# Kernel tuning notes

Measured on AMD Instinct MI355X. Metric: run time of the kernel, lower is better.

Reference implementation:

```python
import jax, jax.numpy as jnp
import numpy as np

D = 2048
N_HID = 512
ATT = 512
BATCH = 256
L = 196


def setup_inputs() -> dict:
    key = jax.random.key(0)
    ks = jax.random.split(key, 8)
    s = 0.02
    return {
        "feature": jax.random.normal(ks[0], (BATCH, L, D), dtype=jnp.float32),
        "prev_h": jax.random.normal(ks[1], (BATCH, N_HID), dtype=jnp.float32),
        "W_enc": jax.random.normal(ks[2], (D, ATT), dtype=jnp.float32) * s,
        "b_enc": jnp.zeros((ATT,), dtype=jnp.float32),
        "W_dec": jax.random.normal(ks[3], (N_HID, ATT), dtype=jnp.float32) * s,
        "b_dec": jnp.zeros((ATT,), dtype=jnp.float32),
        "W_tot": jax.random.normal(ks[4], (ATT, 1), dtype=jnp.float32) * s,
        "b_tot": jnp.zeros((1,), dtype=jnp.float32),
    }


def reference(feature, prev_h, W_enc, b_enc, W_dec, b_dec, W_tot, b_tot):
    # att1: (N, L, A); att2: (N, A)
    att1 = jnp.einsum("nld,da->nla", feature, W_enc) + b_enc
    att2 = prev_h @ W_dec + b_dec
    att = jax.nn.relu(att1 + att2[:, None, :])          # (N, L, A)
    scores = (att @ W_tot)[..., 0] + b_tot[0]           # (N, L)
    alpha = jax.nn.softmax(scores, axis=1)              # (N, L)
    weighted_feature = jnp.einsum("nld,nl->nd", feature, alpha)  # (N, D)
    return weighted_feature, alpha
```

## Files before the change

kernel.cpp:

```cpp
#include <hip/hip_runtime.h>
#include <hip/hip_bf16.h>


typedef unsigned short u16;
typedef __attribute__((ext_vector_type(8))) short short8;
typedef __attribute__((ext_vector_type(4))) float f32x4;

#define BATCH 256
#define LQ    196
#define DDIM  2048
#define ADIM  512
#define MTOT  (BATCH * LQ)
#define WF_N  (BATCH * DDIM)
#define KQP   1032

__device__ __forceinline__ u16 bfc(float f) {
  return __builtin_bit_cast(u16, (__bf16)f);
}

__device__ __forceinline__ ushort4 cvt4(float4 f) {
  ushort4 r;
  r.x = bfc(f.x); r.y = bfc(f.y); r.z = bfc(f.z); r.w = bfc(f.w);
  return r;
}

__device__ __forceinline__ void glds16(const u16* g, u16* l) {
  __builtin_amdgcn_global_load_lds(
      (const __attribute__((address_space(1))) unsigned int*)g,
      (__attribute__((address_space(3))) unsigned int*)l, 16, 0, 0);
}

__global__ void prep_k(const float* __restrict__ W_enc, u16* __restrict__ Bst,
                       const float* __restrict__ prev_h,
                       const float* __restrict__ W_dec,
                       const float* __restrict__ b_dec,
                       const float* __restrict__ b_enc,
                       float* __restrict__ att2,
                       float* __restrict__ scores) {
  const int b = blockIdx.x, tid = threadIdx.x;
  __shared__ u16 smem[32 * 520];
  if (b < 64) {
    const int ks = b;
    for (int i4 = tid; i4 < 4096; i4 += 256) {
      int dl = i4 >> 7;
      int nn = (i4 & 127) << 2;
      float4 f = *(const float4*)(W_enc + (size_t)(ks * 32 + dl) * 512 + nn);
      *(ushort4*)(&smem[dl * 520 + nn]) = cvt4(f);
    }
    __syncthreads();
    for (int idx = tid; idx < 16384; idx += 256) {
      int kq = idx >> 12;
      int n  = (idx >> 3) & 511;
      int e  = idx & 7;
      Bst[(size_t)ks * 16384 + idx] = smem[(kq * 8 + e) * 520 + n];
    }
  } else if (b < 576) {
    const int n  = (b - 64) >> 1;
    const int c0 = ((b - 64) & 1) << 8;
    float* ph = (float*)smem;
    ph[tid]       = prev_h[n * 512 + tid];
    ph[tid + 256] = prev_h[n * 512 + tid + 256];
    __syncthreads();
    float a0 = b_dec[c0 + tid] + b_enc[c0 + tid];
    #pragma unroll 8
    for (int h = 0; h < 512; h++)
      a0 = fmaf(ph[h], W_dec[h * 512 + c0 + tid], a0);
    att2[n * 512 + c0 + tid] = a0;
  } else {
    scores[(b - 576) * 256 + tid] = 0.f;
  }
}

__global__ __launch_bounds__(256, 3) void score_gemm_k(
    const float* __restrict__ feature, const u16* __restrict__ Bst,
    const float* __restrict__ att2, const float* __restrict__ W_tot,
    float* __restrict__ scores) {
  __shared__ __align__(16) u16 sA[2][4 * KQP];
  __shared__ __align__(16) u16 sB[4][4 * KQP];
  __shared__ float sRed[2][128];

  const int tid = threadIdx.x;
  const int b = blockIdx.x;
  const int mt = (b >> 5) * 8 + (b & 7);
  const int nt = (b >> 3) & 3;
  const int r0 = mt << 7, n0 = nt << 7;
  const int wid = tid >> 6, lane = tid & 63;
  const int wgm = wid >> 1, wgn = wid & 1;
  const int quad = lane >> 4, cid = lane & 15;

  const int arow = tid >> 3, akk4 = tid & 7;
  const float* gA = feature + (size_t)(r0 + arow) * 2048 + akk4 * 4;
  const int wAoff = (akk4 >> 1) * KQP + (arow << 3) + ((akk4 & 1) << 2);

  const u16* gBlane = Bst + (size_t)wid * 4096 + ((size_t)n0 << 3) + lane * 8;

  const int abase = quad * KQP + (((wgm << 6) + cid) << 3);
  const int bbase = quad * KQP + (((wgn << 6) + cid) << 3);

  f32x4 zero = {0.f, 0.f, 0.f, 0.f};
  f32x4 acc[4][4];
  #pragma unroll
  for (int i = 0; i < 4; i++)
    #pragma unroll
    for (int j = 0; j < 4; j++) acc[i][j] = zero;

  float4 aS0_0, aS0_1, aS0_2, aS0_3;
  float4 aS1_0, aS1_1, aS1_2, aS1_3;
  float4 aS2_0, aS2_1, aS2_2, aS2_3;

#define LOAD_A(SET, KS) do {                                              \
    const float* p_ = gA + (size_t)(KS) * 32;                             \
    aS##SET##_0 = *(const float4*)(p_);                                   \
    aS##SET##_1 = *(const float4*)(p_ + 32 * 2048);                       \
    aS##SET##_2 = *(const float4*)(p_ + 64 * 2048);                       \
    aS##SET##_3 = *(const float4*)(p_ + 96 * 2048);                       \
  } while (0)

#define STAGE_A(SET, ABUF) do {                                           \
    u16* wa_ = &sA[ABUF][wAoff];                                          \
    *(ushort4*)(wa_)       = cvt4(aS##SET##_0);                           \
    *(ushort4*)(wa_ + 256) = cvt4(aS##SET##_1);                           \
    *(ushort4*)(wa_ + 512) = cvt4(aS##SET##_2);                           \
    *(ushort4*)(wa_ + 768) = cvt4(aS##SET##_3);                           \
  } while (0)

#define GLDS_B2(KS, BUFI) do {                                            \
    const u16* src_ = gBlane + (size_t)(KS) * 16384;                      \
    u16* dst_ = &sB[BUFI][wid * KQP];                                     \
    glds16(src_, dst_);                                                   \
    glds16(src_ + 512, dst_ + 512);                                       \
  } while (0)

#define COMPUTE(ABUF, BBUF) do {                                          \
    const u16* sa_ = &sA[ABUF][abase];                                    \
    const u16* sb_ = &sB[BBUF][bbase];                                    \
    short8 af_[4], bf_[4];                                                \
    _Pragma("unroll")                                                     \
    for (int mi = 0; mi < 4; mi++)                                        \
      af_[mi] = *(const short8*)(sa_ + (mi << 7));                        \
    _Pragma("unroll")                                                     \
    for (int ni = 0; ni < 4; ni++)                                        \
      bf_[ni] = *(const short8*)(sb_ + (ni << 7));                        \
    _Pragma("unroll")                                                     \
    for (int mi = 0; mi < 4; mi++)                                        \
      _Pragma("unroll")                                                   \
      for (int ni = 0; ni < 4; ni++)                                      \
        acc[mi][ni] = __builtin_amdgcn_mfma_f32_16x16x32_bf16(            \
            af_[mi], bf_[ni], acc[mi][ni], 0, 0, 0);                      \
  } while (0)

#define ITER_BODY(KS, SET, ABUF, BRD, BWR) do {                           \
    STAGE_A(SET, ABUF);                                                   \
    GLDS_B2((KS) + 2, BWR);                                               \
    LOAD_A(SET, (KS) + 3);                                                \
    asm volatile("s_waitcnt vmcnt(16) lgkmcnt(0)" ::: "memory");          \
    __builtin_amdgcn_s_barrier();                                         \
    COMPUTE(ABUF, BRD);                                                   \
  } while (0)

  GLDS_B2(0, 0);
  GLDS_B2(1, 1);
  LOAD_A(0, 0);
  LOAD_A(1, 1);
  LOAD_A(2, 2);

  #pragma unroll 1
  for (int kb = 0; kb < 60; kb += 12) {
    ITER_BODY(kb + 0,  0, 0, 0, 2);
    ITER_BODY(kb + 1,  1, 1, 1, 3);
    ITER_BODY(kb + 2,  2, 0, 2, 0);
    ITER_BODY(kb + 3,  0, 1, 3, 1);
    ITER_BODY(kb + 4,  1, 0, 0, 2);
    ITER_BODY(kb + 5,  2, 1, 1, 3);
    ITER_BODY(kb + 6,  0, 0, 2, 0);
    ITER_BODY(kb + 7,  1, 1, 3, 1);
    ITER_BODY(kb + 8,  2, 0, 0, 2);
    ITER_BODY(kb + 9,  0, 1, 1, 3);
    ITER_BODY(kb + 10, 1, 0, 2, 0);
    ITER_BODY(kb + 11, 2, 1, 3, 1);
  }
  ITER_BODY(60, 0, 0, 0, 2);

  STAGE_A(1, 1); GLDS_B2(63, 3); __syncthreads(); COMPUTE(1, 1);
  STAGE_A(2, 0);                 __syncthreads(); COMPUTE(0, 2);
  STAGE_A(0, 1);                 __syncthreads(); COMPUTE(1, 3);

#undef ITER_BODY
#undef COMPUTE
#undef GLDS_B2
#undef STAGE_A
#undef LOAD_A

  float wt[4];
  #pragma unroll
  for (int ni = 0; ni < 4; ni++)
    wt[ni] = W_tot[n0 + (wgn << 6) + ni * 16 + cid];

  #pragma unroll
  for (int mi = 0; mi < 4; mi++) {
    #pragma unroll
    for (int reg = 0; reg < 4; reg++) {
      int row_local = (wgm << 6) + mi * 16 + quad * 4 + reg;
      int row_flat = r0 + row_local;
      int nb = row_flat / 196;
      const float* a2r = att2 + nb * 512 + n0 + (wgn << 6);
      float s = 0.f;
      #pragma unroll
      for (int ni = 0; ni < 4; ni++) {
        float v = acc[mi][ni][reg] + a2r[ni * 16 + cid];
        s += fmaxf(v, 0.f) * wt[ni];
      }
      s += __shfl_xor(s, 1); s += __shfl_xor(s, 2);
      s += __shfl_xor(s, 4); s += __shfl_xor(s, 8);
      if (cid == 0) sRed[wgn][row_local] = s;
    }
  }
  __syncthreads();
  if (tid < 128) atomicAdd(&scores[r0 + tid], sRed[0][tid] + sRed[1][tid]);
}

__global__ void softmax_k(const float* __restrict__ scores,
                          float* __restrict__ alpha) {
  const int n = blockIdx.x, tid = threadIdx.x;
  __shared__ float red[8];
  float s = (tid < LQ) ? scores[n * LQ + tid] : -1e30f;
  float m = s;
  for (int o = 32; o; o >>= 1) m = fmaxf(m, __shfl_xor(m, o));
  if ((tid & 63) == 0) red[tid >> 6] = m;
  __syncthreads();
  m = fmaxf(fmaxf(red[0], red[1]), fmaxf(red[2], red[3]));
  float e = (tid < LQ) ? __expf(s - m) : 0.f;
  float t = e;
  for (int o = 32; o; o >>= 1) t += __shfl_xor(t, o);
  if ((tid & 63) == 0) red[4 + (tid >> 6)] = t;
  __syncthreads();
  t = red[4] + red[5] + red[6] + red[7];
  if (tid < LQ) alpha[n * LQ + tid] = e / t;
}

__global__ void wsum_k(const float* __restrict__ feature,
                       const float* __restrict__ alpha,
                       float* __restrict__ out) {
  const int n = blockIdx.x >> 1, half = blockIdx.x & 1;
  const int tid = threadIdx.x;
  __shared__ float al[LQ];
  if (tid < LQ) al[tid] = alpha[n * LQ + tid];
  __syncthreads();
  const float* fp = feature + (size_t)n * LQ * DDIM + half * 1024 + tid * 4;
  float4 acc = {0.f, 0.f, 0.f, 0.f};
  #pragma unroll 8
  for (int l = 0; l < LQ; l++) {
    float a = al[l];
    float4 f = *(const float4*)(fp + (size_t)l * DDIM);
    acc.x = fmaf(a, f.x, acc.x); acc.y = fmaf(a, f.y, acc.y);
    acc.z = fmaf(a, f.z, acc.z); acc.w = fmaf(a, f.w, acc.w);
  }
  *(float4*)(out + n * DDIM + half * 1024 + tid * 4) = acc;
}

extern "C" void kernel_launch(void* const* d_in, const int* in_sizes, int n_in,
                              void* d_out, int out_size, void* d_ws, size_t ws_size,
                              hipStream_t stream) {
  const float* feature = (const float*)d_in[0];
  const float* prev_h  = (const float*)d_in[1];
  const float* W_enc   = (const float*)d_in[2];
  const float* b_enc   = (const float*)d_in[3];
  const float* W_dec   = (const float*)d_in[4];
  const float* b_dec   = (const float*)d_in[5];
  const float* W_tot   = (const float*)d_in[6];

  float* out   = (float*)d_out;
  float* wf    = out;
  float* alpha = out + WF_N;

  char* ws = (char*)d_ws;
  u16*   Bst    = (u16*)ws;
  float* att2   = (float*)(ws + (2u << 20));
  float* scores = (float*)(ws + (2u << 20) + (512u << 10));

  prep_k<<<772, 256, 0, stream>>>(W_enc, Bst, prev_h, W_dec, b_dec, b_enc,
                                  att2, scores);
  score_gemm_k<<<1568, 256, 0, stream>>>(feature, Bst, att2, W_tot, scores);
  softmax_k<<<256, 256, 0, stream>>>(scores, alpha);
  wsum_k<<<512, 256, 0, stream>>>(feature, alpha, wf);
}
```

Measured before the change: 935.0 us.

## Shorten score GEMM pipeline to double-buffered B and two A register sets

Restructures the K-loop pipeline of the score GEMM. The B tile buffer drops from four LDS stages to two and the A register prefetch from three sets to two. The barrier now comes before issuing the next B global-to-LDS copy, so the copy overlaps the MFMA compute of the current stage. This cuts LDS use and registers, which can raise occupancy, but it reduces prefetch depth and could expose more global memory latency.

Result: faster. 779.7 us (-16.6%).

```diff
diff --git a/kernel.cpp b/kernel.cpp
--- a/kernel.cpp
+++ b/kernel.cpp
@@ -76,7 +76,7 @@
     const float* __restrict__ att2, const float* __restrict__ W_tot,
     float* __restrict__ scores) {
   __shared__ __align__(16) u16 sA[2][4 * KQP];
-  __shared__ __align__(16) u16 sB[4][4 * KQP];
+  __shared__ __align__(16) u16 sB[2][4 * KQP];
   __shared__ float sRed[2][128];
 
   const int tid = threadIdx.x;
@@ -106,7 +106,8 @@
 
   float4 aS0_0, aS0_1, aS0_2, aS0_3;
   float4 aS1_0, aS1_1, aS1_2, aS1_3;
-  float4 aS2_0, aS2_1, aS2_2, aS2_3;
+
+#define FENCE asm volatile("" ::: "memory")
 
 #define LOAD_A(SET, KS) do {                                              \
     const float* p_ = gA + (size_t)(KS) * 32;                             \
@@ -124,7 +125,7 @@
     *(ushort4*)(wa_ + 768) = cvt4(aS##SET##_3);                           \
   } while (0)
 
-#define GLDS_B2(KS, BUFI) do {                                            \
+#define GLDS_B(KS, BUFI) do {                                             \
     const u16* src_ = gBlane + (size_t)(KS) * 16384;                      \
     u16* dst_ = &sB[BUFI][wid * KQP];                                     \
     glds16(src_, dst_);                                                   \
@@ -149,47 +150,41 @@
             af_[mi], bf_[ni], acc[mi][ni], 0, 0, 0);                      \
   } while (0)
 
-#define ITER_BODY(KS, SET, ABUF, BRD, BWR) do {                           \
-    STAGE_A(SET, ABUF);                                                   \
-    GLDS_B2((KS) + 2, BWR);                                               \
-    LOAD_A(SET, (KS) + 3);                                                \
-    asm volatile("s_waitcnt vmcnt(16) lgkmcnt(0)" ::: "memory");          \
-    __builtin_amdgcn_s_barrier();                                         \
-    COMPUTE(ABUF, BRD);                                                   \
-  } while (0)
-
-  GLDS_B2(0, 0);
-  GLDS_B2(1, 1);
+#define ITER(KS, P) do {                                                  \
+    STAGE_A(P, P);                                                        \
+    asm volatile("s_waitcnt vmcnt(4) lgkmcnt(0)\n\ts_barrier"             \
+                 ::: "memory");                                           \
+    GLDS_B((KS) + 1, (P) ^ 1);                                            \
+    FENCE;                                                                \
+    LOAD_A(P, (KS) + 2);                                                  \
+    COMPUTE(P, P);                                                        \
+  } while (0)
+
+  GLDS_B(0, 0);
+  FENCE;
   LOAD_A(0, 0);
   LOAD_A(1, 1);
-  LOAD_A(2, 2);
 
   #pragma unroll 1
-  for (int kb = 0; kb < 60; kb += 12) {
-    ITER_BODY(kb + 0,  0, 0, 0, 2);
-    ITER_BODY(kb + 1,  1, 1, 1, 3);
-    ITER_BODY(kb + 2,  2, 0, 2, 0);
-    ITER_BODY(kb + 3,  0, 1, 3, 1);
-    ITER_BODY(kb + 4,  1, 0, 0, 2);
-    ITER_BODY(kb + 5,  2, 1, 1, 3);
-    ITER_BODY(kb + 6,  0, 0, 2, 0);
-    ITER_BODY(kb + 7,  1, 1, 3, 1);
-    ITER_BODY(kb + 8,  2, 0, 0, 2);
-    ITER_BODY(kb + 9,  0, 1, 1, 3);
-    ITER_BODY(kb + 10, 1, 0, 2, 0);
-    ITER_BODY(kb + 11, 2, 1, 3, 1);
-  }
-  ITER_BODY(60, 0, 0, 0, 2);
-
-  STAGE_A(1, 1); GLDS_B2(63, 3); __syncthreads(); COMPUTE(1, 1);
-  STAGE_A(2, 0);                 __syncthreads(); COMPUTE(0, 2);
-  STAGE_A(0, 1);                 __syncthreads(); COMPUTE(1, 3);
-
-#undef ITER_BODY
+  for (int ks = 0; ks < 62; ks += 2) {
+    ITER(ks, 0);
+    ITER(ks + 1, 1);
+  }
+  STAGE_A(0, 0);
+  asm volatile("s_waitcnt vmcnt(4) lgkmcnt(0)\n\ts_barrier" ::: "memory");
+  GLDS_B(63, 1);
+  FENCE;
+  COMPUTE(0, 0);
+  STAGE_A(1, 1);
+  asm volatile("s_waitcnt vmcnt(0) lgkmcnt(0)\n\ts_barrier" ::: "memory");
+  COMPUTE(1, 1);
+
+#undef ITER
 #undef COMPUTE
-#undef GLDS_B2
+#undef GLDS_B
 #undef STAGE_A
 #undef LOAD_A
+#undef FENCE
 
   float wt[4];
   #pragma unroll
```
